# Kernel tuning notes

Measured on AMD Instinct MI355X. Metric: run time of the kernel, lower is better.

The kernel has to match this reference:

```python
import jax, jax.numpy as jnp
import numpy as np

TOP_K = 2  # config.n_expert_capacity


def setup_inputs() -> dict:
    key = jax.random.key(0)
    k1, k2, k3, k4 = jax.random.split(key, 4)
    B, S, D, F, E = 2, 2048, 1024, 4096, 8
    x = jax.random.normal(k1, (B, S, D), dtype=jnp.float32)
    # kaiming-ish scaling so router logits / activations stay well-conditioned
    choice = jax.random.normal(k2, (E, D), dtype=jnp.float32) / np.sqrt(D)
    W1 = jax.random.normal(k3, (E, D, F), dtype=jnp.float32) / np.sqrt(D)
    W2 = jax.random.normal(k4, (E, F, D), dtype=jnp.float32) / np.sqrt(F)
    return {"x": x, "choice": choice, "W1": W1, "W2": W2}


def reference(x, choice, W1, W2):
    B, S, D = x.shape
    E = choice.shape[0]
    # Router: softmax over experts, then top-k (weights NOT renormalized, per source)
    logits = jnp.einsum('bsd,ed->bse', x, choice)          # [B,S,E]
    weights = jax.nn.softmax(logits, axis=-1)
    k_w, k_idx = jax.lax.top_k(weights, TOP_K)             # [B,S,K]
    # Dense combine weights: zero for non-selected experts -> same math as scatter/gather
    cw = jnp.sum(jax.nn.one_hot(k_idx, E, dtype=x.dtype) * k_w[..., None], axis=-2)  # [B,S,E]
    xt = x.reshape(B * S, D)
    cwt = cw.reshape(B * S, E)
    y = jnp.zeros_like(xt)
    for e in range(E):  # small fixed expert loop; avoids [T,E,F] intermediate
        h = jax.nn.silu(xt @ W1[e]) @ W2[e]                # [T,D]
        y = y + cwt[:, e:e+1] * h
    # dropout p=0.0 / eval mode -> identity
    return y.reshape(B, S, D)
```

## Files before the change

### kernel.cpp

```cpp
#include <hip/hip_runtime.h>
#include <hip/hip_fp16.h>
#include <cmath>

#define T_TOKENS 4096
#define DDIM     1024
#define FDIM     4096
#define NEXP     8
#define NPAIR    8192

typedef _Float16 half8  __attribute__((ext_vector_type(8)));
typedef _Float16 half4v __attribute__((ext_vector_type(4)));
typedef float    floatx4 __attribute__((ext_vector_type(4)));

#define GLOAD16(g, l) __builtin_amdgcn_global_load_lds(                     \
    (const __attribute__((address_space(1))) void*)(g),                      \
    (__attribute__((address_space(3))) void*)(l), 16, 0, 0)

static const size_t OFF_XH  = 0;
static const size_t SZ_XH   = (size_t)T_TOKENS * DDIM * 2;
static const size_t OFF_W1T = OFF_XH + SZ_XH;
static const size_t SZ_WT   = (size_t)NEXP * FDIM * DDIM * 2;
static const size_t OFF_W2T = OFF_W1T + SZ_WT;
static const size_t OFF_H   = OFF_W2T + SZ_WT;
static const size_t SZ_H    = (size_t)NPAIR * FDIM * 2;
static const size_t OFF_PT  = OFF_H + SZ_H;
static const size_t OFF_TI  = OFF_PT + NPAIR * 4;
static const size_t OFF_TW  = OFF_TI + NPAIR * 4;
static const size_t OFF_PS  = OFF_TW + NPAIR * 4;
static const size_t OFF_CNT = OFF_PS + NPAIR * 4;
static const size_t OFF_OFS = OFF_CNT + 64;
static const size_t OFF_CUR = OFF_OFS + 64;
static const size_t WS_NEED = OFF_CUR + 64;

__global__ __launch_bounds__(256)
void router_kernel(const float* __restrict__ x, const float* __restrict__ choice,
                   _Float16* __restrict__ xh, int* __restrict__ top_idx,
                   float* __restrict__ top_w, int* __restrict__ counts)
{
    __shared__ float ch[NEXP * DDIM];
    for (int i = threadIdx.x * 4; i < NEXP * DDIM; i += 256 * 4) {
        *(float4*)&ch[i] = *(const float4*)&choice[i];
    }
    __syncthreads();

    const int lane = threadIdx.x & 63;
    const int wv   = threadIdx.x >> 6;
    const int t    = blockIdx.x * 4 + wv;

    const float* xp = x + (size_t)t * DDIM;
    float4 xr[4];
#pragma unroll
    for (int p = 0; p < 4; ++p) xr[p] = *(const float4*)(xp + p * 256 + lane * 4);

#pragma unroll
    for (int p = 0; p < 4; ++p) {
        half4v hv = { (_Float16)xr[p].x, (_Float16)xr[p].y,
                      (_Float16)xr[p].z, (_Float16)xr[p].w };
        *(half4v*)(xh + (size_t)t * DDIM + p * 256 + lane * 4) = hv;
    }

    float lg[NEXP];
#pragma unroll
    for (int e = 0; e < NEXP; ++e) {
        float s = 0.f;
#pragma unroll
        for (int p = 0; p < 4; ++p) {
            float4 c4 = *(float4*)&ch[e * DDIM + p * 256 + lane * 4];
            s += xr[p].x * c4.x + xr[p].y * c4.y + xr[p].z * c4.z + xr[p].w * c4.w;
        }
#pragma unroll
        for (int o = 32; o; o >>= 1) s += __shfl_xor(s, o, 64);
        lg[e] = s;
    }

    if (lane == 0) {
        float mx = lg[0];
#pragma unroll
        for (int e = 1; e < NEXP; ++e) mx = fmaxf(mx, lg[e]);
        float w[NEXP]; float sum = 0.f;
#pragma unroll
        for (int e = 0; e < NEXP; ++e) { w[e] = expf(lg[e] - mx); sum += w[e]; }
        float inv = 1.f / sum;
#pragma unroll
        for (int e = 0; e < NEXP; ++e) w[e] *= inv;
        int i0 = 0; float w0 = w[0];
#pragma unroll
        for (int e = 1; e < NEXP; ++e) if (w[e] > w0) { w0 = w[e]; i0 = e; }
        int i1 = -1; float w1 = -1.f;
#pragma unroll
        for (int e = 0; e < NEXP; ++e) if (e != i0 && w[e] > w1) { w1 = w[e]; i1 = e; }
        top_idx[t * 2 + 0] = i0;  top_w[t * 2 + 0] = w0;
        top_idx[t * 2 + 1] = i1;  top_w[t * 2 + 1] = w1;
        atomicAdd(&counts[i0], 1);
        atomicAdd(&counts[i1], 1);
    }
}

__global__ void scan_kernel(const int* __restrict__ counts, int* __restrict__ offsets,
                            int* __restrict__ cursors)
{
    if (threadIdx.x == 0) {
        int o = 0;
        for (int e = 0; e < NEXP; ++e) { offsets[e] = o; cursors[e] = o; o += counts[e]; }
        offsets[NEXP] = o;
    }
}

__global__ __launch_bounds__(256)
void fill_kernel(const int* __restrict__ top_idx, const float* __restrict__ top_w,
                 int* __restrict__ cursors, int* __restrict__ pair_tok,
                 int* __restrict__ pslot)
{
    int t = blockIdx.x * 256 + threadIdx.x;
#pragma unroll
    for (int k = 0; k < 2; ++k) {
        int e = top_idx[t * 2 + k];
        int pos = atomicAdd(&cursors[e], 1);
        pair_tok[pos] = t;
        pslot[t * 2 + k] = pos;
    }
}

__global__ __launch_bounds__(256)
void transpose_cvt(const float* __restrict__ in, _Float16* __restrict__ out, int R, int C)
{
    __shared__ float tile[64][65];
    const int e  = blockIdx.z;
    const float*    ip = in  + ((size_t)e * R + blockIdx.y * 64) * C + blockIdx.x * 64;
    _Float16*       op = out + ((size_t)e * C + blockIdx.x * 64) * R + blockIdx.y * 64;
    const int lr = threadIdx.x >> 4;
    const int lc = (threadIdx.x & 15) * 4;
#pragma unroll
    for (int p = 0; p < 4; ++p) {
        float4 v = *(const float4*)(ip + (size_t)(lr + p * 16) * C + lc);
        tile[lc + 0][lr + p * 16] = v.x;
        tile[lc + 1][lr + p * 16] = v.y;
        tile[lc + 2][lr + p * 16] = v.z;
        tile[lc + 3][lr + p * 16] = v.w;
    }
    __syncthreads();
#pragma unroll
    for (int p = 0; p < 4; ++p) {
        int oc = lr + p * 16;
        half4v hv = { (_Float16)tile[oc][lc + 0], (_Float16)tile[oc][lc + 1],
                      (_Float16)tile[oc][lc + 2], (_Float16)tile[oc][lc + 3] };
        *(half4v*)(op + (size_t)oc * R + lc) = hv;
    }
}

template<bool GATHER, int EPI, int GM, int NB>
__global__ __launch_bounds__(256)
void moe_gemm(const _Float16* __restrict__ Abase, const _Float16* __restrict__ Bt,
              _Float16* __restrict__ Hout, float* __restrict__ H2out,
              const int* __restrict__ pair_tok,
              const int* __restrict__ counts, const int* __restrict__ offsets,
              const int K, const int N)
{
    const int MBSTR = 16;
    const int q  = gridDim.x >> 3;
    const int wg = (blockIdx.x & 7) * q + (blockIdx.x >> 3);
    const int per_e = MBSTR * NB;
    const int e  = wg / per_e;
    int ide = wg - e * per_e;
    const int g = ide / (NB * GM);
    ide -= g * (NB * GM);
    const int nb  = ide / GM;
    const int mb0 = g * GM + (ide - nb * GM);

    const int cnt = counts[e];
    const int off = offsets[e];

    const int tid  = threadIdx.x;
    const int lane = tid & 63;
    const int wv   = tid >> 6;
    const int wm   = wv >> 1, wn = wv & 1;

    __shared__ __align__(16) _Float16 As[2][128 * 64];
    __shared__ __align__(16) _Float16 Bs[2][128 * 64];

    const int crow = lane >> 3;
    const int swz  = ((lane & 7) * 8) ^ (crow << 3);

    const int kc = (lane >> 4) * 8;
    const int fr = lane & 15;
    const int rsw = (fr & 7) << 3;
    const int nK = K >> 6;

    const _Float16* bsrc[4];
#pragma unroll
    for (int i = 0; i < 4; ++i) {
        const int n = nb * 128 + (wv * 4 + i) * 8 + crow;
        bsrc[i] = Bt + ((size_t)e * N + n) * K + swz;
    }

    for (int mb = mb0; mb * 128 < cnt; mb += MBSTR) {
        const _Float16* asrc[4];
#pragma unroll
        for (int i = 0; i < 4; ++i) {
            int r = mb * 128 + (wv * 4 + i) * 8 + crow;
            int pr = off + (r < cnt ? r : cnt - 1);
            long rowi = GATHER ? (long)pair_tok[pr] : (long)pr;
            asrc[i] = Abase + (size_t)rowi * K + swz;
        }

        floatx4 acc[4][4] = {};

#pragma unroll
        for (int i = 0; i < 4; ++i) {
            GLOAD16(asrc[i], &As[0][(wv * 4 + i) * 512]);
            GLOAD16(bsrc[i], &Bs[0][(wv * 4 + i) * 512]);
        }
        __syncthreads();

        int cur = 0;
        for (int kt = 0; kt < nK; ++kt) {
            if (kt + 1 < nK) {
                const int ko = (kt + 1) * 64;
#pragma unroll
                for (int i = 0; i < 4; ++i) {
                    GLOAD16(asrc[i] + ko, &As[cur ^ 1][(wv * 4 + i) * 512]);
                    GLOAD16(bsrc[i] + ko, &Bs[cur ^ 1][(wv * 4 + i) * 512]);
                }
            }
#pragma unroll
            for (int s = 0; s < 2; ++s) {
                const int rc = (s * 32 + kc) ^ rsw;
                half8 af[4], bf[4];
#pragma unroll
                for (int i = 0; i < 4; ++i)
                    af[i] = *(const half8*)&As[cur][(wm * 64 + i * 16 + fr) * 64 + rc];
#pragma unroll
                for (int j = 0; j < 4; ++j)
                    bf[j] = *(const half8*)&Bs[cur][(wn * 64 + j * 16 + fr) * 64 + rc];
#pragma unroll
                for (int i = 0; i < 4; ++i)
#pragma unroll
                    for (int j = 0; j < 4; ++j)
                        acc[i][j] = __builtin_amdgcn_mfma_f32_16x16x32_f16(af[i], bf[j], acc[i][j], 0, 0, 0);
            }
            __syncthreads();
            cur ^= 1;
        }

        const int qr = lane >> 4;
        const int nbase = nb * 128 + wn * 64;
#pragma unroll
        for (int i = 0; i < 4; ++i) {
#pragma unroll
            for (int r = 0; r < 4; ++r) {
                const int gm = mb * 128 + wm * 64 + i * 16 + qr * 4 + r;
                if (gm < cnt) {
                    if (EPI == 0) {
                        const size_t hrow = (size_t)(off + gm) * FDIM;
#pragma unroll
                        for (int j = 0; j < 4; ++j) {
                            float v = acc[i][j][r];
                            v = v / (1.f + expf(-v));
                            Hout[hrow + nbase + j * 16 + fr] = (_Float16)v;
                        }
                    } else {
                        const size_t hrow = (size_t)(off + gm) * DDIM;
#pragma unroll
                        for (int j = 0; j < 4; ++j)
                            H2out[hrow + nbase + j * 16 + fr] = acc[i][j][r];
                    }
                }
            }
        }
    }
}

__global__ __launch_bounds__(256)
void combine_kernel(const float* __restrict__ H2, const int* __restrict__ pslot,
                    const float* __restrict__ top_w, float* __restrict__ y)
{
    const int t  = blockIdx.x;
    const int p0 = pslot[t * 2 + 0], p1 = pslot[t * 2 + 1];
    const float w0 = top_w[t * 2 + 0], w1 = top_w[t * 2 + 1];
    const int d = threadIdx.x * 4;
    float4 a = *(const float4*)&H2[(size_t)p0 * DDIM + d];
    float4 b = *(const float4*)&H2[(size_t)p1 * DDIM + d];
    float4 o = { w0 * a.x + w1 * b.x, w0 * a.y + w1 * b.y,
                 w0 * a.z + w1 * b.z, w0 * a.w + w1 * b.w };
    *(float4*)&y[(size_t)t * DDIM + d] = o;
}

extern "C" void kernel_launch(void* const* d_in, const int* in_sizes, int n_in,
                              void* d_out, int out_size, void* d_ws, size_t ws_size,
                              hipStream_t stream)
{
    const float* x      = (const float*)d_in[0];
    const float* choice = (const float*)d_in[1];
    const float* W1     = (const float*)d_in[2];
    const float* W2     = (const float*)d_in[3];
    float* y = (float*)d_out;

    char* ws = (char*)d_ws;
    if (ws_size < WS_NEED) return;

    _Float16* xh  = (_Float16*)(ws + OFF_XH);
    _Float16* W1T = (_Float16*)(ws + OFF_W1T);
    _Float16* W2T = (_Float16*)(ws + OFF_W2T);
    _Float16* H   = (_Float16*)(ws + OFF_H);
    float*    H2  = (float*)(ws + OFF_W1T);
    int*   pair_tok = (int*)(ws + OFF_PT);
    int*   top_idx  = (int*)(ws + OFF_TI);
    float* top_w    = (float*)(ws + OFF_TW);
    int*   pslot    = (int*)(ws + OFF_PS);
    int*   counts   = (int*)(ws + OFF_CNT);
    int*   offsets  = (int*)(ws + OFF_OFS);
    int*   cursors  = (int*)(ws + OFF_CUR);

    hipMemsetAsync(counts, 0, 192, stream);

    router_kernel<<<T_TOKENS / 4, 256, 0, stream>>>(x, choice, xh, top_idx, top_w, counts);
    scan_kernel<<<1, 64, 0, stream>>>(counts, offsets, cursors);
    fill_kernel<<<T_TOKENS / 256, 256, 0, stream>>>(top_idx, top_w, cursors, pair_tok, pslot);

    transpose_cvt<<<dim3(FDIM / 64, DDIM / 64, NEXP), 256, 0, stream>>>(W1, W1T, DDIM, FDIM);
    transpose_cvt<<<dim3(DDIM / 64, FDIM / 64, NEXP), 256, 0, stream>>>(W2, W2T, FDIM, DDIM);

    moe_gemm<true, 0, 16, FDIM / 128><<<NEXP * 16 * (FDIM / 128), 256, 0, stream>>>(
        xh, W1T, H, nullptr, pair_tok, counts, offsets, DDIM, FDIM);

    moe_gemm<false, 1, 2, DDIM / 128><<<NEXP * 16 * (DDIM / 128), 256, 0, stream>>>(
        H, W2T, nullptr, H2, pair_tok, counts, offsets, FDIM, DDIM);

    combine_kernel<<<T_TOKENS, 256, 0, stream>>>(H2, pslot, top_w, y);
}
```

Measured before the change: 766.3 us.

## Enlarge MoE GEMM tiles to 256x256 with 512 threads and split-K down-projection

Replaces the 128x128 expert GEMM with a 256x256 tile version that runs 8 waves per block and uses 128KB of double-buffered LDS, raising arithmetic intensity per loaded byte. The second GEMM is split in two along K, writing two partial H2 buffers. The combine kernel now sums those partials before applying the router weights. This trades lower occupancy, one block per CU with a large accumulator, and extra H2 traffic for fewer global loads per MFMA.

Result: no change. 760.6 us (-0.7%).

```diff
diff --git a/kernel.cpp b/kernel.cpp
--- a/kernel.cpp
+++ b/kernel.cpp
@@ -148,24 +148,23 @@
     }
 }
 
-template<bool GATHER, int EPI, int GM, int NB>
-__global__ __launch_bounds__(256)
-void moe_gemm(const _Float16* __restrict__ Abase, const _Float16* __restrict__ Bt,
-              _Float16* __restrict__ Hout, float* __restrict__ H2out,
-              const int* __restrict__ pair_tok,
-              const int* __restrict__ counts, const int* __restrict__ offsets,
-              const int K, const int N)
-{
-    const int MBSTR = 16;
+template<bool GATHER, int EPI, int NB, int NKS>
+__global__ __launch_bounds__(512, 1)
+void moe_gemm256(const _Float16* __restrict__ Abase, const _Float16* __restrict__ Bt,
+                 _Float16* __restrict__ Hout, float* __restrict__ H2out,
+                 const int* __restrict__ pair_tok,
+                 const int* __restrict__ counts, const int* __restrict__ offsets,
+                 const int Kfull, const int N)
+{
     const int q  = gridDim.x >> 3;
     const int wg = (blockIdx.x & 7) * q + (blockIdx.x >> 3);
-    const int per_e = MBSTR * NB;
+    const int per_e = 4 * NB * NKS;
     const int e  = wg / per_e;
     int ide = wg - e * per_e;
-    const int g = ide / (NB * GM);
-    ide -= g * (NB * GM);
-    const int nb  = ide / GM;
-    const int mb0 = g * GM + (ide - nb * GM);
+    const int nb   = ide / (4 * NKS);
+    int rem  = ide - nb * (4 * NKS);
+    const int ks   = rem >> 2;
+    const int slot = rem & 3;
 
     const int cnt = counts[e];
     const int off = offsets[e];
@@ -173,10 +172,10 @@
     const int tid  = threadIdx.x;
     const int lane = tid & 63;
     const int wv   = tid >> 6;
-    const int wm   = wv >> 1, wn = wv & 1;
-
-    __shared__ __align__(16) _Float16 As[2][128 * 64];
-    __shared__ __align__(16) _Float16 Bs[2][128 * 64];
+    const int wm   = wv >> 2, wn = wv & 3;
+
+    __shared__ __align__(16) _Float16 As[2][256 * 64];
+    __shared__ __align__(16) _Float16 Bs[2][256 * 64];
 
     const int crow = lane >> 3;
     const int swz  = ((lane & 7) * 8) ^ (crow << 3);
@@ -184,26 +183,29 @@
     const int kc = (lane >> 4) * 8;
     const int fr = lane & 15;
     const int rsw = (fr & 7) << 3;
-    const int nK = K >> 6;
+
+    const int Kloc = Kfull / NKS;
+    const int k0   = ks * Kloc;
+    const int nK   = Kloc >> 6;
 
     const _Float16* bsrc[4];
 #pragma unroll
     for (int i = 0; i < 4; ++i) {
-        const int n = nb * 128 + (wv * 4 + i) * 8 + crow;
-        bsrc[i] = Bt + ((size_t)e * N + n) * K + swz;
-    }
-
-    for (int mb = mb0; mb * 128 < cnt; mb += MBSTR) {
+        const int n = nb * 256 + (wv * 4 + i) * 8 + crow;
+        bsrc[i] = Bt + ((size_t)e * N + n) * Kfull + k0 + swz;
+    }
+
+    for (int mb = slot; mb * 256 < cnt; mb += 4) {
         const _Float16* asrc[4];
 #pragma unroll
         for (int i = 0; i < 4; ++i) {
-            int r = mb * 128 + (wv * 4 + i) * 8 + crow;
+            int r = mb * 256 + (wv * 4 + i) * 8 + crow;
             int pr = off + (r < cnt ? r : cnt - 1);
             long rowi = GATHER ? (long)pair_tok[pr] : (long)pr;
-            asrc[i] = Abase + (size_t)rowi * K + swz;
-        }
-
-        floatx4 acc[4][4] = {};
+            asrc[i] = Abase + (size_t)rowi * Kfull + k0 + swz;
+        }
+
+        floatx4 acc[8][4] = {};
 
 #pragma unroll
         for (int i = 0; i < 4; ++i) {
@@ -225,15 +227,15 @@
 #pragma unroll
             for (int s = 0; s < 2; ++s) {
                 const int rc = (s * 32 + kc) ^ rsw;
-                half8 af[4], bf[4];
-#pragma unroll
-                for (int i = 0; i < 4; ++i)
-                    af[i] = *(const half8*)&As[cur][(wm * 64 + i * 16 + fr) * 64 + rc];
+                half8 af[8], bf[4];
+#pragma unroll
+                for (int i = 0; i < 8; ++i)
+                    af[i] = *(const half8*)&As[cur][(wm * 128 + i * 16 + fr) * 64 + rc];
 #pragma unroll
                 for (int j = 0; j < 4; ++j)
                     bf[j] = *(const half8*)&Bs[cur][(wn * 64 + j * 16 + fr) * 64 + rc];
 #pragma unroll
-                for (int i = 0; i < 4; ++i)
+                for (int i = 0; i < 8; ++i)
 #pragma unroll
                     for (int j = 0; j < 4; ++j)
                         acc[i][j] = __builtin_amdgcn_mfma_f32_16x16x32_f16(af[i], bf[j], acc[i][j], 0, 0, 0);
@@ -243,12 +245,12 @@
         }
 
         const int qr = lane >> 4;
-        const int nbase = nb * 128 + wn * 64;
-#pragma unroll
-        for (int i = 0; i < 4; ++i) {
+        const int nbase = nb * 256 + wn * 64;
+#pragma unroll
+        for (int i = 0; i < 8; ++i) {
 #pragma unroll
             for (int r = 0; r < 4; ++r) {
-                const int gm = mb * 128 + wm * 64 + i * 16 + qr * 4 + r;
+                const int gm = mb * 256 + wm * 128 + i * 16 + qr * 4 + r;
                 if (gm < cnt) {
                     if (EPI == 0) {
                         const size_t hrow = (size_t)(off + gm) * FDIM;
@@ -259,7 +261,7 @@
                             Hout[hrow + nbase + j * 16 + fr] = (_Float16)v;
                         }
                     } else {
-                        const size_t hrow = (size_t)(off + gm) * DDIM;
+                        const size_t hrow = ((size_t)ks * NPAIR + off + gm) * DDIM;
 #pragma unroll
                         for (int j = 0; j < 4; ++j)
                             H2out[hrow + nbase + j * 16 + fr] = acc[i][j][r];
@@ -278,10 +280,14 @@
     const int p0 = pslot[t * 2 + 0], p1 = pslot[t * 2 + 1];
     const float w0 = top_w[t * 2 + 0], w1 = top_w[t * 2 + 1];
     const int d = threadIdx.x * 4;
-    float4 a = *(const float4*)&H2[(size_t)p0 * DDIM + d];
-    float4 b = *(const float4*)&H2[(size_t)p1 * DDIM + d];
-    float4 o = { w0 * a.x + w1 * b.x, w0 * a.y + w1 * b.y,
-                 w0 * a.z + w1 * b.z, w0 * a.w + w1 * b.w };
+    float4 a0 = *(const float4*)&H2[(size_t)p0 * DDIM + d];
+    float4 a1 = *(const float4*)&H2[((size_t)NPAIR + p0) * DDIM + d];
+    float4 b0 = *(const float4*)&H2[(size_t)p1 * DDIM + d];
+    float4 b1 = *(const float4*)&H2[((size_t)NPAIR + p1) * DDIM + d];
+    float4 o = { w0 * (a0.x + a1.x) + w1 * (b0.x + b1.x),
+                 w0 * (a0.y + a1.y) + w1 * (b0.y + b1.y),
+                 w0 * (a0.z + a1.z) + w1 * (b0.z + b1.z),
+                 w0 * (a0.w + a1.w) + w1 * (b0.w + b1.w) };
     *(float4*)&y[(size_t)t * DDIM + d] = o;
 }
 
@@ -320,10 +326,10 @@
     transpose_cvt<<<dim3(FDIM / 64, DDIM / 64, NEXP), 256, 0, stream>>>(W1, W1T, DDIM, FDIM);
     transpose_cvt<<<dim3(DDIM / 64, FDIM / 64, NEXP), 256, 0, stream>>>(W2, W2T, FDIM, DDIM);
 
-    moe_gemm<true, 0, 16, FDIM / 128><<<NEXP * 16 * (FDIM / 128), 256, 0, stream>>>(
+    moe_gemm256<true, 0, FDIM / 256, 1><<<NEXP * 4 * (FDIM / 256), 512, 0, stream>>>(
         xh, W1T, H, nullptr, pair_tok, counts, offsets, DDIM, FDIM);
 
-    moe_gemm<false, 1, 2, DDIM / 128><<<NEXP * 16 * (DDIM / 128), 256, 0, stream>>>(
+    moe_gemm256<false, 1, DDIM / 256, 2><<<NEXP * 4 * (DDIM / 256) * 2, 512, 0, stream>>>(
         H, W2T, nullptr, H2, pair_tok, counts, offsets, FDIM, DDIM);
 
     combine_kernel<<<T_TOKENS, 256, 0, stream>>>(H2, pslot, top_w, y);
```
